# Optimization experiments

Hardware: AMD Instinct MI355X
Metric: run time of the kernel (lower is better)

## Reference

```python
import jax, jax.numpy as jnp
import numpy as np

N_EMBD = 1024
HEAD_SIZE = 128

def setup_inputs() -> dict:
    key = jax.random.key(0)
    k1, k2, k3, k4 = jax.random.split(key, 4)
    x = jax.random.normal(k1, (8, 2048, N_EMBD), dtype=jnp.float32)
    # Linear(n_embd, head_size, bias=False): y = x @ W, W: [n_embd, head_size]
    s = 1.0 / np.sqrt(N_EMBD)
    Wk = jax.random.uniform(k2, (N_EMBD, HEAD_SIZE), jnp.float32, -s, s)
    Wq = jax.random.uniform(k3, (N_EMBD, HEAD_SIZE), jnp.float32, -s, s)
    Wv = jax.random.uniform(k4, (N_EMBD, HEAD_SIZE), jnp.float32, -s, s)
    return {"x": x, "Wk": Wk, "Wq": Wq, "Wv": Wv}

def reference(x, Wk, Wq, Wv):
    B, T, C = x.shape
    H = Wk.shape[1]
    k = jnp.einsum('btc,ch->bth', x, Wk)
    q = jnp.einsum('btc,ch->bth', x, Wq)
    v = jnp.einsum('btc,ch->bth', x, Wv)
    # scores [B, T, T], causal mask, scaled by head_size**-0.5
    wei = jnp.einsum('bqh,bkh->bqk', q, k) * (H ** -0.5)
    causal = jnp.tril(jnp.ones((T, T), dtype=bool))
    wei = jnp.where(causal, wei, -jnp.inf)
    wei = jax.nn.softmax(wei, axis=-1)
    # dropout p=0.0 (eval mode): identity
    out = jnp.einsum('bqk,bkh->bqh', wei, v)
    return out
```

## Files before the change

### kernel.cpp

```cpp
#include <hip/hip_runtime.h>
#include <hip/hip_bf16.h>
#include <stdint.h>

typedef short v8s __attribute__((ext_vector_type(8)));
typedef float v4f __attribute__((ext_vector_type(4)));
typedef float v16f __attribute__((ext_vector_type(16)));

#define N_EMBD 1024
#define HEAD 128
#define TOKENS 16384
#define T_SEQ 2048
#define BATCH 8
#define BPB 96

__device__ __forceinline__ short f2bf(float f) {
    union { float f; uint32_t u; } c; c.f = f;
    uint32_t u = c.u;
    uint32_t r = (u + 0x7fffu + ((u >> 16) & 1u)) >> 16;
    return (short)r;
}

__device__ __forceinline__ float bf2f(short s) {
    union { uint32_t u; float f; } c; c.u = ((uint32_t)(uint16_t)s) << 16;
    return c.f;
}

__global__ __launch_bounds__(256)
void wt_kernel(const float* __restrict__ Wq, const float* __restrict__ Wk,
               const float* __restrict__ Wv, short* __restrict__ wt) {
    int tid = blockIdx.x * 256 + threadIdx.x;
    int w   = tid >> 17;
    int rem = tid & 131071;
    int c = rem >> 7, h = rem & 127;
    const float* src = (w == 0) ? Wq : ((w == 1) ? Wk : Wv);
    wt[w * 131072 + h * 1024 + c] = f2bf(src[rem]);
}

__global__ __launch_bounds__(256)
void qkv_gemm(const float* __restrict__ x, const short* __restrict__ wt,
              short* __restrict__ qkv, short* __restrict__ vT) {
    const int bid = blockIdx.x;
    const int xcd = bid & 7, q = bid >> 3;
    const int mt  = xcd * 32 + q / 3;
    const int w   = q % 3;
    const int m0  = mt * 64;

    __shared__ short smem[2][64 * 40 + 128 * 40];

    const int t = threadIdx.x;
    const int lane = t & 63, wv = t >> 6;
    const int l31 = lane & 31, l1 = lane >> 5;
    const int wm = wv & 1, wn = wv >> 1;

    const short* wtw = wt + w * 131072;

    const int arow = t >> 3, ac4 = t & 7;
    const int brow = t >> 2, bc8 = t & 3;
    const float* aptr0 = x + (size_t)(m0 + arow) * 1024 + ac4 * 4;
    const float* aptr1 = x + (size_t)(m0 + arow + 32) * 1024 + ac4 * 4;
    const short* bptr0 = wtw + brow * 1024 + bc8 * 8;
    const short* bptr1 = wtw + (brow + 64) * 1024 + bc8 * 8;

    float4 af0 = *(const float4*)aptr0;
    float4 af1 = *(const float4*)aptr1;
    uint4  bf0 = *(const uint4*)bptr0;
    uint4  bf1 = *(const uint4*)bptr1;

    v16f acc[2];
    for (int i = 0; i < 16; ++i) { acc[0][i] = 0.f; acc[1][i] = 0.f; }

    {
        short* sA = smem[0]; short* sB = smem[0] + 64 * 40;
        union { short s[4]; uint64_t u; } p0, p1;
        p0.s[0] = f2bf(af0.x); p0.s[1] = f2bf(af0.y); p0.s[2] = f2bf(af0.z); p0.s[3] = f2bf(af0.w);
        p1.s[0] = f2bf(af1.x); p1.s[1] = f2bf(af1.y); p1.s[2] = f2bf(af1.z); p1.s[3] = f2bf(af1.w);
        *(uint64_t*)(&sA[arow * 40 + ac4 * 4]) = p0.u;
        *(uint64_t*)(&sA[(arow + 32) * 40 + ac4 * 4]) = p1.u;
        *(uint4*)(&sB[brow * 40 + bc8 * 8]) = bf0;
        *(uint4*)(&sB[(brow + 64) * 40 + bc8 * 8]) = bf1;
    }

    for (int it = 0; it < 32; ++it) {
        if (it < 31) {
            int kk = (it + 1) * 32;
            af0 = *(const float4*)(aptr0 + kk);
            af1 = *(const float4*)(aptr1 + kk);
            bf0 = *(const uint4*)(bptr0 + kk);
            bf1 = *(const uint4*)(bptr1 + kk);
        }
        __syncthreads();
        const short* sA = smem[it & 1];
        const short* sB = smem[it & 1] + 64 * 40;
        for (int ks = 0; ks < 2; ++ks) {
            v8s a = *(const v8s*)&sA[(wm * 32 + l31) * 40 + ks * 16 + l1 * 8];
            for (int ni = 0; ni < 2; ++ni) {
                v8s b = *(const v8s*)&sB[(wn * 64 + ni * 32 + l31) * 40 + ks * 16 + l1 * 8];
                acc[ni] = __builtin_amdgcn_mfma_f32_32x32x16_bf16(a, b, acc[ni], 0, 0, 0);
            }
        }
        if (it < 31) {
            short* nA = smem[(it + 1) & 1];
            short* nB = smem[(it + 1) & 1] + 64 * 40;
            union { short s[4]; uint64_t u; } p0, p1;
            p0.s[0] = f2bf(af0.x); p0.s[1] = f2bf(af0.y); p0.s[2] = f2bf(af0.z); p0.s[3] = f2bf(af0.w);
            p1.s[0] = f2bf(af1.x); p1.s[1] = f2bf(af1.y); p1.s[2] = f2bf(af1.z); p1.s[3] = f2bf(af1.w);
            *(uint64_t*)(&nA[arow * 40 + ac4 * 4]) = p0.u;
            *(uint64_t*)(&nA[(arow + 32) * 40 + ac4 * 4]) = p1.u;
            *(uint4*)(&nB[brow * 40 + bc8 * 8]) = bf0;
            *(uint4*)(&nB[(brow + 64) * 40 + bc8 * 8]) = bf1;
        }
    }

    if (w < 2) {
        short* outw = qkv + (size_t)w * TOKENS * HEAD;
        for (int ni = 0; ni < 2; ++ni) {
            int col = wn * 64 + ni * 32 + l31;
            for (int reg = 0; reg < 16; ++reg) {
                int m = (reg & 3) + 8 * (reg >> 2) + 4 * l1;
                outw[(size_t)(m0 + wm * 32 + m) * HEAD + col] = f2bf(acc[ni][reg]);
            }
        }
    } else {
        __syncthreads();
        short* sT = (short*)smem;
        for (int ni = 0; ni < 2; ++ni) {
            int col = wn * 64 + ni * 32 + l31;
            for (int g = 0; g < 4; ++g) {
                union { short s[4]; uint64_t u; } pk;
                for (int r = 0; r < 4; ++r) pk.s[r] = f2bf(acc[ni][g * 4 + r]);
                *(uint64_t*)(&sT[col * 72 + wm * 32 + 8 * g + 4 * l1]) = pk.u;
            }
        }
        __syncthreads();
        for (int it = 0; it < 4; ++it) {
            int c = it * 256 + t;
            int col = c >> 3, c8 = c & 7;
            uint4 d = *(const uint4*)(&sT[col * 72 + c8 * 8]);
            *(uint4*)(&vT[(size_t)col * TOKENS + m0 + c8 * 8]) = d;
        }
    }
}

__global__ __launch_bounds__(256)
void attn_kernel(const short* __restrict__ qb, const short* __restrict__ kb,
                 const short* __restrict__ vT, short* __restrict__ po,
                 float* __restrict__ pl) {
    const int bid = blockIdx.x;
    const int b  = bid & 7;
    const int r0 = bid >> 3;
    int qt2 = 0, c0 = 0;
    for (;;) { int sz = (2 * qt2 + 4) / 3; if (r0 < c0 + sz) break; c0 += sz; ++qt2; }
    const int s = r0 - c0;
    const int q0 = qt2 * 128;
    const int nkt = 2 * qt2 + 2;
    const int kt0 = s * 3;
    const int kt1 = (kt0 + 3 < nkt) ? (kt0 + 3) : nkt;

    __shared__ short sK[64 * 128];
    __shared__ short sV[128 * 64];
    __shared__ short sP[128 * 72];

    const int t = threadIdx.x;
    const int wv = t >> 6, lane = t & 63, ln = lane & 15, qd = lane >> 4;
    const int wrow0 = q0 + wv * 32;

    v8s qf[2][4];
    for (int qg = 0; qg < 2; ++qg) {
        const short* qrow = qb + ((size_t)(b * T_SEQ + wrow0 + qg * 16 + ln)) * HEAD;
        for (int ks = 0; ks < 4; ++ks)
            qf[qg][ks] = *(const v8s*)(qrow + ks * 32 + qd * 8);
    }

    v4f o[2][8] = {};
    float rs[2] = {0.f, 0.f};
    const float sc = 1.4426950408889634f / 11.313708498984761f;

    for (int kt = kt0; kt < kt1; ++kt) {
        __syncthreads();
        const short* kbase = kb + ((size_t)(b * T_SEQ + kt * 64)) * HEAD;
        for (int it = 0; it < 4; ++it) {
            int c = it * 256 + t;
            int row = c >> 4, ch = c & 15;
            uint4 d = *(const uint4*)(kbase + row * HEAD + ch * 8);
            int sch = (ch & 8) | ((ch ^ row) & 7);
            *(uint4*)(&sK[row * 128 + sch * 8]) = d;
        }
        const short* vbase = vT + (size_t)(b * T_SEQ + kt * 64);
        for (int it = 0; it < 4; ++it) {
            int c = it * 256 + t;
            int dd = c >> 3, ch = c & 7;
            uint4 d = *(const uint4*)(vbase + (size_t)dd * TOKENS + ch * 8);
            *(uint4*)(&sV[dd * 64 + ((ch ^ dd) & 7) * 8]) = d;
        }
        __syncthreads();

        if (kt * 64 >= wrow0 + 32) continue;

        v4f st[2][4] = {};
        for (int ni = 0; ni < 4; ++ni) {
            int krow = ni * 16 + ln;
            for (int ks = 0; ks < 4; ++ks) {
                int ch = ks * 4 + qd;
                v8s kf = *(const v8s*)&sK[krow * 128 + ((ch & 8) | ((ch ^ krow) & 7)) * 8];
                st[0][ni] = __builtin_amdgcn_mfma_f32_16x16x32_bf16(kf, qf[0][ks], st[0][ni], 0, 0, 0);
                st[1][ni] = __builtin_amdgcn_mfma_f32_16x16x32_bf16(kf, qf[1][ks], st[1][ni], 0, 0, 0);
            }
        }

        const bool needMask = (kt * 64 + 63 > wrow0);
        for (int qg = 0; qg < 2; ++qg) {
            int prow = wv * 32 + qg * 16 + ln;
            int qrow_g = wrow0 + qg * 16 + ln;
            for (int ni = 0; ni < 4; ++ni) {
                union { short s[4]; uint64_t u; } pk;
                for (int r = 0; r < 4; ++r) {
                    float p = exp2f(st[qg][ni][r] * sc);
                    int kg = kt * 64 + ni * 16 + qd * 4 + r;
                    if (needMask && kg > qrow_g) p = 0.f;
                    rs[qg] += p;
                    pk.s[r] = f2bf(p);
                }
                *(uint64_t*)(&sP[prow * 72 + ni * 16 + qd * 4]) = pk.u;
            }
        }

        for (int kk2 = 0; kk2 < 2; ++kk2) {
            v8s pf0 = *(const v8s*)&sP[(wv * 32 + ln) * 72 + kk2 * 32 + qd * 8];
            v8s pf1 = *(const v8s*)&sP[(wv * 32 + 16 + ln) * 72 + kk2 * 32 + qd * 8];
            for (int oni = 0; oni < 8; ++oni) {
                int dd = oni * 16 + ln;
                int ch = kk2 * 4 + qd;
                v8s vf = *(const v8s*)&sV[dd * 64 + ((ch ^ dd) & 7) * 8];
                o[0][oni] = __builtin_amdgcn_mfma_f32_16x16x32_bf16(vf, pf0, o[0][oni], 0, 0, 0);
                o[1][oni] = __builtin_amdgcn_mfma_f32_16x16x32_bf16(vf, pf1, o[1][oni], 0, 0, 0);
            }
        }
    }

    float lsum[2];
    for (int qg = 0; qg < 2; ++qg) {
        float v = rs[qg];
        v += __shfl_xor(v, 16);
        v += __shfl_xor(v, 32);
        lsum[qg] = v;
    }

    short* pob = po + (size_t)bid * 128 * 128;
    for (int qg = 0; qg < 2; ++qg)
        for (int oni = 0; oni < 8; ++oni) {
            union { short s[4]; uint2 u; } pk;
            for (int r = 0; r < 4; ++r) pk.s[r] = f2bf(o[qg][oni][r]);
            *(uint2*)(&pob[(((qg * 8 + oni) * 4 + wv) * 64 + lane) * 4]) = pk.u;
        }
    if (lane < 16)
        for (int qg = 0; qg < 2; ++qg)
            pl[bid * 128 + wv * 32 + qg * 16 + lane] = lsum[qg];
}

__global__ __launch_bounds__(256)
void combine_kernel(const short* __restrict__ po, const float* __restrict__ pl,
                    float* __restrict__ out) {
    const int bid = blockIdx.x;
    const int dh  = bid & 1;
    const int qh  = (bid >> 1) & 1;
    const int qt2 = (bid >> 2) & 15;
    const int b   = bid >> 6;
    int cum = 0;
    for (int j = 0; j < qt2; ++j) cum += (2 * j + 4) / 3;
    const int S = (2 * qt2 + 4) / 3;

    const int t = threadIdx.x;
    const int wv = t >> 6, lane = t & 63, ln = lane & 15, qd = lane >> 4;

    float l = 0.f;
    float accv[4][4] = {};

    for (int si = 0; si < S; ++si) {
        int slot = (cum + si) * 8 + b;
        l += pl[slot * 128 + wv * 32 + qh * 16 + ln];
        const short* pob = po + (size_t)slot * 16384;
        for (int oi = 0; oi < 4; ++oi) {
            int oni = dh * 4 + oi;
            union { short s[4]; uint2 u; } pk;
            pk.u = *(const uint2*)(&pob[(((qh * 8 + oni) * 4 + wv) * 64 + lane) * 4]);
            for (int r = 0; r < 4; ++r) accv[oi][r] += bf2f(pk.s[r]);
        }
    }
    float inv = 1.f / l;
    float* ob = out + ((size_t)(b * T_SEQ) + qt2 * 128 + wv * 32 + qh * 16 + ln) * HEAD;
    for (int oi = 0; oi < 4; ++oi) {
        float4 o4 = make_float4(accv[oi][0] * inv, accv[oi][1] * inv,
                                accv[oi][2] * inv, accv[oi][3] * inv);
        *(float4*)(ob + (dh * 4 + oi) * 16 + qd * 4) = o4;
    }
}

extern "C" void kernel_launch(void* const* d_in, const int* in_sizes, int n_in,
                              void* d_out, int out_size, void* d_ws, size_t ws_size,
                              hipStream_t stream) {
    const float* x  = (const float*)d_in[0];
    const float* Wk = (const float*)d_in[1];
    const float* Wq = (const float*)d_in[2];
    const float* Wv = (const float*)d_in[3];
    float* out = (float*)d_out;

    char* ws = (char*)d_ws;
    short* wt = (short*)ws;
    short* qb = (short*)(ws + 0x100000u);
    short* kb = (short*)(ws + 0x500000u);
    short* vT = (short*)(ws + 0x900000u);
    short* po = (short*)(ws + 0xD00000u);
    float* pl = (float*)(ws + 0x2500000u);
    short* qkv = qb;

    wt_kernel<<<1536, 256, 0, stream>>>(Wq, Wk, Wv, wt);
    qkv_gemm<<<768, 256, 0, stream>>>(x, wt, qkv, vT);
    attn_kernel<<<BATCH * BPB, 256, 0, stream>>>(qb, kb, vT, po, pl);
    combine_kernel<<<512, 256, 0, stream>>>(po, pl, out);
}
```

Measured before the change: 168.7 us.

## Load QKV GEMM operands straight from global into registers, skipping LDS staging

The QKV projection GEMM no longer stages A and B tiles through double-buffered shared memory. Each lane loads its MFMA fragments directly from global memory into registers, with a two-deep register prefetch. The A operand is converted to bf16 in registers, and the launch bounds now ask for 3 blocks per CU. This removes LDS traffic and the per-iteration __syncthreads, but each x element is now loaded by both wn-waves and each weight fragment by both wm-waves, with less coalesced access patterns.

```diff
diff --git a/kernel.cpp b/kernel.cpp
--- a/kernel.cpp
+++ b/kernel.cpp
@@ -23,6 +23,13 @@
 __device__ __forceinline__ float bf2f(short s) {
     union { uint32_t u; float f; } c; c.u = ((uint32_t)(uint16_t)s) << 16;
     return c.f;
+}
+
+__device__ __forceinline__ v8s pack8(float4 lo, float4 hi) {
+    v8s r;
+    r[0] = f2bf(lo.x); r[1] = f2bf(lo.y); r[2] = f2bf(lo.z); r[3] = f2bf(lo.w);
+    r[4] = f2bf(hi.x); r[5] = f2bf(hi.y); r[6] = f2bf(hi.z); r[7] = f2bf(hi.w);
+    return r;
 }
 
 __global__ __launch_bounds__(256)
@@ -36,7 +43,7 @@
     wt[w * 131072 + h * 1024 + c] = f2bf(src[rem]);
 }
 
-__global__ __launch_bounds__(256)
+__global__ __launch_bounds__(256, 3)
 void qkv_gemm(const float* __restrict__ x, const short* __restrict__ wt,
               short* __restrict__ qkv, short* __restrict__ vT) {
     const int bid = blockIdx.x;
@@ -45,7 +52,7 @@
     const int w   = q % 3;
     const int m0  = mt * 64;
 
-    __shared__ short smem[2][64 * 40 + 128 * 40];
+    __shared__ short sT[128 * 72];
 
     const int t = threadIdx.x;
     const int lane = t & 63, wv = t >> 6;
@@ -54,62 +61,71 @@
 
     const short* wtw = wt + w * 131072;
 
-    const int arow = t >> 3, ac4 = t & 7;
-    const int brow = t >> 2, bc8 = t & 3;
-    const float* aptr0 = x + (size_t)(m0 + arow) * 1024 + ac4 * 4;
-    const float* aptr1 = x + (size_t)(m0 + arow + 32) * 1024 + ac4 * 4;
-    const short* bptr0 = wtw + brow * 1024 + bc8 * 8;
-    const short* bptr1 = wtw + (brow + 64) * 1024 + bc8 * 8;
-
-    float4 af0 = *(const float4*)aptr0;
-    float4 af1 = *(const float4*)aptr1;
-    uint4  bf0 = *(const uint4*)bptr0;
-    uint4  bf1 = *(const uint4*)bptr1;
+    const float* ap  = x   + (size_t)(m0 + wm * 32 + l31) * 1024 + l1 * 8;
+    const short* bp0 = wtw + (wn * 64 + l31) * 1024 + l1 * 8;
+    const short* bp1 = wtw + (wn * 64 + 32 + l31) * 1024 + l1 * 8;
 
     v16f acc[2];
     for (int i = 0; i < 16; ++i) { acc[0][i] = 0.f; acc[1][i] = 0.f; }
 
-    {
-        short* sA = smem[0]; short* sB = smem[0] + 64 * 40;
-        union { short s[4]; uint64_t u; } p0, p1;
-        p0.s[0] = f2bf(af0.x); p0.s[1] = f2bf(af0.y); p0.s[2] = f2bf(af0.z); p0.s[3] = f2bf(af0.w);
-        p1.s[0] = f2bf(af1.x); p1.s[1] = f2bf(af1.y); p1.s[2] = f2bf(af1.z); p1.s[3] = f2bf(af1.w);
-        *(uint64_t*)(&sA[arow * 40 + ac4 * 4]) = p0.u;
-        *(uint64_t*)(&sA[(arow + 32) * 40 + ac4 * 4]) = p1.u;
-        *(uint4*)(&sB[brow * 40 + bc8 * 8]) = bf0;
-        *(uint4*)(&sB[(brow + 64) * 40 + bc8 * 8]) = bf1;
-    }
-
-    for (int it = 0; it < 32; ++it) {
-        if (it < 31) {
-            int kk = (it + 1) * 32;
-            af0 = *(const float4*)(aptr0 + kk);
-            af1 = *(const float4*)(aptr1 + kk);
-            bf0 = *(const uint4*)(bptr0 + kk);
-            bf1 = *(const uint4*)(bptr1 + kk);
-        }
-        __syncthreads();
-        const short* sA = smem[it & 1];
-        const short* sB = smem[it & 1] + 64 * 40;
-        for (int ks = 0; ks < 2; ++ks) {
-            v8s a = *(const v8s*)&sA[(wm * 32 + l31) * 40 + ks * 16 + l1 * 8];
-            for (int ni = 0; ni < 2; ++ni) {
-                v8s b = *(const v8s*)&sB[(wn * 64 + ni * 32 + l31) * 40 + ks * 16 + l1 * 8];
-                acc[ni] = __builtin_amdgcn_mfma_f32_32x32x16_bf16(a, b, acc[ni], 0, 0, 0);
-            }
-        }
-        if (it < 31) {
-            short* nA = smem[(it + 1) & 1];
-            short* nB = smem[(it + 1) & 1] + 64 * 40;
-            union { short s[4]; uint64_t u; } p0, p1;
-            p0.s[0] = f2bf(af0.x); p0.s[1] = f2bf(af0.y); p0.s[2] = f2bf(af0.z); p0.s[3] = f2bf(af0.w);
-            p1.s[0] = f2bf(af1.x); p1.s[1] = f2bf(af1.y); p1.s[2] = f2bf(af1.z); p1.s[3] = f2bf(af1.w);
-            *(uint64_t*)(&nA[arow * 40 + ac4 * 4]) = p0.u;
-            *(uint64_t*)(&nA[(arow + 32) * 40 + ac4 * 4]) = p1.u;
-            *(uint4*)(&nB[brow * 40 + bc8 * 8]) = bf0;
-            *(uint4*)(&nB[(brow + 64) * 40 + bc8 * 8]) = bf1;
-        }
-    }
+    float4 A0k0l, A0k0h, A0k1l, A0k1h, A1k0l, A1k0h, A1k1l, A1k1h;
+    v8s    B0k0n0, B0k0n1, B0k1n0, B0k1n1, B1k0n0, B1k0n1, B1k1n0, B1k1n1;
+
+#define LOADSET0(IT) do { int kk_ = (IT) * 32;                                   \
+        A0k0l = *(const float4*)(ap + kk_);                                      \
+        A0k0h = *(const float4*)(ap + kk_ + 4);                                  \
+        A0k1l = *(const float4*)(ap + kk_ + 16);                                 \
+        A0k1h = *(const float4*)(ap + kk_ + 20);                                 \
+        B0k0n0 = *(const v8s*)(bp0 + kk_);                                       \
+        B0k0n1 = *(const v8s*)(bp1 + kk_);                                       \
+        B0k1n0 = *(const v8s*)(bp0 + kk_ + 16);                                  \
+        B0k1n1 = *(const v8s*)(bp1 + kk_ + 16);                                  \
+    } while (0)
+
+#define LOADSET1(IT) do { int kk_ = (IT) * 32;                                   \
+        A1k0l = *(const float4*)(ap + kk_);                                      \
+        A1k0h = *(const float4*)(ap + kk_ + 4);                                  \
+        A1k1l = *(const float4*)(ap + kk_ + 16);                                 \
+        A1k1h = *(const float4*)(ap + kk_ + 20);                                 \
+        B1k0n0 = *(const v8s*)(bp0 + kk_);                                       \
+        B1k0n1 = *(const v8s*)(bp1 + kk_);                                       \
+        B1k1n0 = *(const v8s*)(bp0 + kk_ + 16);                                  \
+        B1k1n1 = *(const v8s*)(bp1 + kk_ + 16);                                  \
+    } while (0)
+
+#define COMPUTE0() do {                                                          \
+        v8s a_;                                                                  \
+        a_ = pack8(A0k0l, A0k0h);                                                \
+        acc[0] = __builtin_amdgcn_mfma_f32_32x32x16_bf16(a_, B0k0n0, acc[0], 0, 0, 0); \
+        acc[1] = __builtin_amdgcn_mfma_f32_32x32x16_bf16(a_, B0k0n1, acc[1], 0, 0, 0); \
+        a_ = pack8(A0k1l, A0k1h);                                                \
+        acc[0] = __builtin_amdgcn_mfma_f32_32x32x16_bf16(a_, B0k1n0, acc[0], 0, 0, 0); \
+        acc[1] = __builtin_amdgcn_mfma_f32_32x32x16_bf16(a_, B0k1n1, acc[1], 0, 0, 0); \
+    } while (0)
+
+#define COMPUTE1() do {                                                          \
+        v8s a_;                                                                  \
+        a_ = pack8(A1k0l, A1k0h);                                                \
+        acc[0] = __builtin_amdgcn_mfma_f32_32x32x16_bf16(a_, B1k0n0, acc[0], 0, 0, 0); \
+        acc[1] = __builtin_amdgcn_mfma_f32_32x32x16_bf16(a_, B1k0n1, acc[1], 0, 0, 0); \
+        a_ = pack8(A1k1l, A1k1h);                                                \
+        acc[0] = __builtin_amdgcn_mfma_f32_32x32x16_bf16(a_, B1k1n0, acc[0], 0, 0, 0); \
+        acc[1] = __builtin_amdgcn_mfma_f32_32x32x16_bf16(a_, B1k1n1, acc[1], 0, 0, 0); \
+    } while (0)
+
+    LOADSET0(0);
+    LOADSET1(1);
+    for (int it = 0; it < 32; it += 2) {
+        COMPUTE0();
+        if (it + 2 < 32) LOADSET0(it + 2);
+        COMPUTE1();
+        if (it + 3 < 32) LOADSET1(it + 3);
+    }
+
+#undef LOADSET0
+#undef LOADSET1
+#undef COMPUTE0
+#undef COMPUTE1
 
     if (w < 2) {
         short* outw = qkv + (size_t)w * TOKENS * HEAD;
@@ -122,7 +138,6 @@
         }
     } else {
         __syncthreads();
-        short* sT = (short*)smem;
         for (int ni = 0; ni < 2; ++ni) {
             int col = wn * 64 + ni * 32 + l31;
             for (int g = 0; g < 4; ++g) {
```

Measured after the change: 217.6 us. 29.0% more time.
